# Performance work log

Measured on AMD Instinct MI355X. Metric: run time of the kernel, lower is better.

Reference implementation:

```python
import jax, jax.numpy as jnp
import numpy as np

SLOT_DIM = 256
HIDDEN = 128
NUM_REL = 8


def setup_inputs() -> dict:
    key = jax.random.key(0)
    ks = jax.random.split(key, 5)
    B, N, D = 8, 256, SLOT_DIM
    slots = jax.random.normal(ks[0], (B, N, D), dtype=jnp.float32)
    # Linear(2D -> H): store as [2D, H] (x @ W + b)
    s1 = 1.0 / np.sqrt(2 * D)
    W1 = jax.random.uniform(ks[1], (2 * D, HIDDEN), jnp.float32, -s1, s1)
    b1 = jax.random.uniform(ks[2], (HIDDEN,), jnp.float32, -s1, s1)
    s2 = 1.0 / np.sqrt(HIDDEN)
    W2 = jax.random.uniform(ks[3], (HIDDEN, NUM_REL), jnp.float32, -s2, s2)
    b2 = jax.random.uniform(ks[4], (NUM_REL,), jnp.float32, -s2, s2)
    return {"slots": slots, "W1": W1, "b1": b1, "W2": W2, "b2": b2}


def reference(slots, W1, b1, W2, b2):
    # cat([slots_i, slots_j]) @ W1 == slots_i @ W1[:D] + slots_j @ W1[D:]
    # so project each slot once, then broadcast-add over the pair grid.
    D = slots.shape[-1]
    proj_i = jnp.einsum("bnd,dh->bnh", slots, W1[:D])   # [B,N,H]
    proj_j = jnp.einsum("bnd,dh->bnh", slots, W1[D:])   # [B,N,H]
    h = proj_i[:, :, None, :] + proj_j[:, None, :, :] + b1  # [B,N,N,H]
    h = jax.nn.relu(h)
    logits = jnp.einsum("bijh,hr->bijr", h, W2) + b2     # [B,N,N,R]
    return jax.nn.sigmoid(logits)
```

## Files before the change

kernel.cpp:

```cpp
#include <hip/hip_runtime.h>
#include <hip/hip_fp16.h>
#include <math.h>

#define BATCH 8
#define NSLOT 256
#define DDIM  256
#define HID   128
#define NREL  8

typedef _Float16 half8 __attribute__((ext_vector_type(8)));
typedef float float4v __attribute__((ext_vector_type(4)));

union U8 {
  uint32_t u[4];
  _Float16 f[8];
  half8 v;
  float4 f4;
};

union H4 {
  _Float16 f[4];
  double d;
};


__global__ __launch_bounds__(256) void wt_kernel(
    const float* __restrict__ W1, _Float16* __restrict__ WT) {
  __shared__ float T[32][33];
  const int tx = threadIdx.x & 31;
  const int ty = threadIdx.x >> 5;
  const int c0 = blockIdx.x * 32, k0 = blockIdx.y * 32;
#pragma unroll
  for (int p = 0; p < 4; ++p) {
    const int k = k0 + ty + p * 8;
    const int c = c0 + tx;
    T[ty + p * 8][tx] = (c < HID) ? W1[(size_t)k * HID + c]
                                  : W1[(size_t)(DDIM + k) * HID + (c - HID)];
  }
  __syncthreads();
#pragma unroll
  for (int p = 0; p < 4; ++p) {
    const int cl = ty + p * 8;
    WT[(size_t)(c0 + cl) * 256 + k0 + tx] = (_Float16)T[tx][cl];
  }
}

__global__ __launch_bounds__(256, 4) void fused_kernel(
    const float* __restrict__ slots, const _Float16* __restrict__ WT,
    const float* __restrict__ b1, const float* __restrict__ W2,
    const float* __restrict__ b2, float* __restrict__ out) {
  __shared__ _Float16 LB[48 * 264];
  _Float16* SLI = LB;
  _Float16* SLJ = LB + 16 * 264;
  _Float16* P1L = LB;
  _Float16* P2L = LB + 16 * 136;

  const int tid  = threadIdx.x;
  const int w    = tid >> 6;
  const int lane = tid & 63;
  const int lo16 = lane & 15;
  const int kg   = lane >> 4;

  const int b  = blockIdx.z;
  const int i0 = blockIdx.y * 16;
  const int j0 = blockIdx.x * 32;
  const float* Sb = slots + (size_t)b * NSLOT * DDIM;

#pragma unroll
  for (int p = 0; p < 4; ++p) {
    const int idx = tid + p * 256;
    const int r  = idx >> 6;
    const int c4 = (idx & 63) * 4;
    const float4 f = *(const float4*)(Sb + (size_t)(i0 + r) * DDIM + c4);
    H4 h;
    h.f[0] = (_Float16)f.x; h.f[1] = (_Float16)f.y;
    h.f[2] = (_Float16)f.z; h.f[3] = (_Float16)f.w;
    *(double*)&SLI[r * 264 + c4] = h.d;
  }
#pragma unroll
  for (int p = 0; p < 8; ++p) {
    const int idx = tid + p * 256;
    const int r  = idx >> 6;
    const int c4 = (idx & 63) * 4;
    const float4 f = *(const float4*)(Sb + (size_t)(j0 + r) * DDIM + c4);
    H4 h;
    h.f[0] = (_Float16)f.x; h.f[1] = (_Float16)f.y;
    h.f[2] = (_Float16)f.z; h.f[3] = (_Float16)f.w;
    *(double*)&SLJ[r * 264 + c4] = h.d;
  }
  __syncthreads();

  float4v p1acc[2];
  float4v p2acc[2][2];
  float b1v[2];
#pragma unroll
  for (int t = 0; t < 2; ++t) {
    p1acc[t] = (float4v){0.0f, 0.0f, 0.0f, 0.0f};
    p2acc[t][0] = (float4v){0.0f, 0.0f, 0.0f, 0.0f};
    p2acc[t][1] = (float4v){0.0f, 0.0f, 0.0f, 0.0f};
  }
#pragma unroll
  for (int t = 0; t < 2; ++t) {
    const int c = (2 * w + t) * 16 + lo16;
    b1v[t] = b1[c];
    U8 bf1[8], bf2[8];
#pragma unroll
    for (int ks = 0; ks < 8; ++ks) {
      bf1[ks].f4 = *(const float4*)(WT + (size_t)c * 256 + ks * 32 + kg * 8);
      bf2[ks].f4 = *(const float4*)(WT + (size_t)(HID + c) * 256 + ks * 32 + kg * 8);
    }
#pragma unroll
    for (int ks = 0; ks < 8; ++ks) {
      U8 a;
      a.f4 = *(const float4*)&SLI[lo16 * 264 + ks * 32 + kg * 8];
      p1acc[t] = __builtin_amdgcn_mfma_f32_16x16x32_f16(a.v, bf1[ks].v, p1acc[t], 0, 0, 0);
    }
#pragma unroll
    for (int mt = 0; mt < 2; ++mt) {
#pragma unroll
      for (int ks = 0; ks < 8; ++ks) {
        U8 a;
        a.f4 = *(const float4*)&SLJ[(mt * 16 + lo16) * 264 + ks * 32 + kg * 8];
        p2acc[t][mt] =
            __builtin_amdgcn_mfma_f32_16x16x32_f16(a.v, bf2[ks].v, p2acc[t][mt], 0, 0, 0);
      }
    }
  }
  __syncthreads();

#pragma unroll
  for (int t = 0; t < 2; ++t) {
    const int col = (2 * w + t) * 16 + lo16;
#pragma unroll
    for (int reg = 0; reg < 4; ++reg) {
      P1L[(kg * 4 + reg) * 136 + col] = (_Float16)(p1acc[t][reg] + b1v[t]);
      P2L[(kg * 4 + reg) * 136 + col] = (_Float16)p2acc[t][0][reg];
      P2L[(16 + kg * 4 + reg) * 136 + col] = (_Float16)p2acc[t][1][reg];
    }
  }
  __syncthreads();

  const int n  = lo16;
  const int jw = w & 1;
  const int ih = w >> 1;

  U8 w2f[4];
#pragma unroll
  for (int kq = 0; kq < 4; ++kq) {
#pragma unroll
    for (int u = 0; u < 8; ++u) {
      const int k = kq * 32 + kg * 8 + u;
      w2f[kq].f[u] = (n < 8) ? (_Float16)W2[k * NREL + n] : (_Float16)0.0f;
    }
  }
  const float b2v = (n < 8) ? b2[n] : 0.0f;

  U8 pj[4];
#pragma unroll
  for (int kq = 0; kq < 4; ++kq) {
    pj[kq].f4 = *(const float4*)&P2L[(jw * 16 + n) * 136 + kq * 32 + kg * 8];
  }

#pragma unroll
  for (int i = 0; i < 8; ++i) {
    const int ii = ih * 8 + i;
    float4v acc = {0.0f, 0.0f, 0.0f, 0.0f};
#pragma unroll
    for (int kq = 0; kq < 4; ++kq) {
      U8 pi;
      pi.f4 = *(const float4*)&P1L[ii * 136 + kq * 32 + kg * 8];
      U8 h;
      h.v = __builtin_elementwise_max(pj[kq].v + pi.v, (half8)(_Float16)0.0f);
      acc = __builtin_amdgcn_mfma_f32_16x16x32_f16(h.v, w2f[kq].v, acc, 0, 0, 0);
    }
    if (n < 8) {
      float* obase =
          out + (((size_t)b * NSLOT + (i0 + ii)) * NSLOT + (j0 + jw * 16)) * NREL + n;
#pragma unroll
      for (int reg = 0; reg < 4; ++reg) {
        const int jrow = kg * 4 + reg;
        const float x = acc[reg] + b2v;
        obase[jrow * NREL] = __builtin_amdgcn_rcpf(1.0f + __expf(-x));
      }
    }
  }
}

extern "C" void kernel_launch(void* const* d_in, const int* in_sizes, int n_in,
                              void* d_out, int out_size, void* d_ws, size_t ws_size,
                              hipStream_t stream) {
  const float* slots = (const float*)d_in[0];
  const float* W1    = (const float*)d_in[1];
  const float* b1    = (const float*)d_in[2];
  const float* W2    = (const float*)d_in[3];
  const float* b2    = (const float*)d_in[4];
  float* out   = (float*)d_out;
  _Float16* WT = (_Float16*)d_ws;

  wt_kernel<<<dim3(8, 8), 256, 0, stream>>>(W1, WT);
  fused_kernel<<<dim3(NSLOT / 32, NSLOT / 16, BATCH), 256, 0, stream>>>(
      slots, WT, b1, W2, b2, out);
}
```

Before: 92.13 us.

## Halve j-tile to 16, double grid, and pre-transpose W2 to fp16

```diff
diff --git a/kernel.cpp b/kernel.cpp
--- a/kernel.cpp
+++ b/kernel.cpp
@@ -25,7 +25,8 @@
 
 
 __global__ __launch_bounds__(256) void wt_kernel(
-    const float* __restrict__ W1, _Float16* __restrict__ WT) {
+    const float* __restrict__ W1, const float* __restrict__ W2,
+    _Float16* __restrict__ WT, _Float16* __restrict__ W2T) {
   __shared__ float T[32][33];
   const int tx = threadIdx.x & 31;
   const int ty = threadIdx.x >> 5;
@@ -43,13 +44,21 @@
     const int cl = ty + p * 8;
     WT[(size_t)(c0 + cl) * 256 + k0 + tx] = (_Float16)T[tx][cl];
   }
+  if (blockIdx.x == 0 && blockIdx.y == 0) {
+#pragma unroll
+    for (int p = 0; p < 8; ++p) {
+      const int idx = threadIdx.x + p * 256;
+      const int n = idx >> 7, k = idx & 127;
+      W2T[n * 128 + k] = (n < 8) ? (_Float16)W2[k * NREL + n] : (_Float16)0.0f;
+    }
+  }
 }
 
 __global__ __launch_bounds__(256, 4) void fused_kernel(
     const float* __restrict__ slots, const _Float16* __restrict__ WT,
-    const float* __restrict__ b1, const float* __restrict__ W2,
+    const _Float16* __restrict__ W2T, const float* __restrict__ b1,
     const float* __restrict__ b2, float* __restrict__ out) {
-  __shared__ _Float16 LB[48 * 264];
+  __shared__ _Float16 LB[32 * 264];
   _Float16* SLI = LB;
   _Float16* SLJ = LB + 16 * 264;
   _Float16* P1L = LB;
@@ -63,41 +72,29 @@
 
   const int b  = blockIdx.z;
   const int i0 = blockIdx.y * 16;
-  const int j0 = blockIdx.x * 32;
+  const int j0 = blockIdx.x * 16;
   const float* Sb = slots + (size_t)b * NSLOT * DDIM;
 
-#pragma unroll
-  for (int p = 0; p < 4; ++p) {
-    const int idx = tid + p * 256;
-    const int r  = idx >> 6;
-    const int c4 = (idx & 63) * 4;
-    const float4 f = *(const float4*)(Sb + (size_t)(i0 + r) * DDIM + c4);
-    H4 h;
-    h.f[0] = (_Float16)f.x; h.f[1] = (_Float16)f.y;
-    h.f[2] = (_Float16)f.z; h.f[3] = (_Float16)f.w;
-    *(double*)&SLI[r * 264 + c4] = h.d;
-  }
 #pragma unroll
   for (int p = 0; p < 8; ++p) {
     const int idx = tid + p * 256;
     const int r  = idx >> 6;
     const int c4 = (idx & 63) * 4;
-    const float4 f = *(const float4*)(Sb + (size_t)(j0 + r) * DDIM + c4);
+    const int grow = (r < 16) ? (i0 + r) : (j0 + r - 16);
+    const float4 f = *(const float4*)(Sb + (size_t)grow * DDIM + c4);
     H4 h;
     h.f[0] = (_Float16)f.x; h.f[1] = (_Float16)f.y;
     h.f[2] = (_Float16)f.z; h.f[3] = (_Float16)f.w;
-    *(double*)&SLJ[r * 264 + c4] = h.d;
+    *(double*)&LB[r * 264 + c4] = h.d;
   }
   __syncthreads();
 
-  float4v p1acc[2];
-  float4v p2acc[2][2];
+  float4v p1acc[2], p2acc[2];
   float b1v[2];
 #pragma unroll
   for (int t = 0; t < 2; ++t) {
     p1acc[t] = (float4v){0.0f, 0.0f, 0.0f, 0.0f};
-    p2acc[t][0] = (float4v){0.0f, 0.0f, 0.0f, 0.0f};
-    p2acc[t][1] = (float4v){0.0f, 0.0f, 0.0f, 0.0f};
+    p2acc[t] = (float4v){0.0f, 0.0f, 0.0f, 0.0f};
   }
 #pragma unroll
   for (int t = 0; t < 2; ++t) {
@@ -116,14 +113,10 @@
       p1acc[t] = __builtin_amdgcn_mfma_f32_16x16x32_f16(a.v, bf1[ks].v, p1acc[t], 0, 0, 0);
     }
 #pragma unroll
-    for (int mt = 0; mt < 2; ++mt) {
-#pragma unroll
-      for (int ks = 0; ks < 8; ++ks) {
-        U8 a;
-        a.f4 = *(const float4*)&SLJ[(mt * 16 + lo16) * 264 + ks * 32 + kg * 8];
-        p2acc[t][mt] =
-            __builtin_amdgcn_mfma_f32_16x16x32_f16(a.v, bf2[ks].v, p2acc[t][mt], 0, 0, 0);
-      }
+    for (int ks = 0; ks < 8; ++ks) {
+      U8 a;
+      a.f4 = *(const float4*)&SLJ[lo16 * 264 + ks * 32 + kg * 8];
+      p2acc[t] = __builtin_amdgcn_mfma_f32_16x16x32_f16(a.v, bf2[ks].v, p2acc[t], 0, 0, 0);
     }
   }
   __syncthreads();
@@ -134,48 +127,37 @@
 #pragma unroll
     for (int reg = 0; reg < 4; ++reg) {
       P1L[(kg * 4 + reg) * 136 + col] = (_Float16)(p1acc[t][reg] + b1v[t]);
-      P2L[(kg * 4 + reg) * 136 + col] = (_Float16)p2acc[t][0][reg];
-      P2L[(16 + kg * 4 + reg) * 136 + col] = (_Float16)p2acc[t][1][reg];
+      P2L[(kg * 4 + reg) * 136 + col] = (_Float16)p2acc[t][reg];
     }
   }
   __syncthreads();
 
-  const int n  = lo16;
-  const int jw = w & 1;
-  const int ih = w >> 1;
-
+  const int n = lo16;
   U8 w2f[4];
 #pragma unroll
-  for (int kq = 0; kq < 4; ++kq) {
-#pragma unroll
-    for (int u = 0; u < 8; ++u) {
-      const int k = kq * 32 + kg * 8 + u;
-      w2f[kq].f[u] = (n < 8) ? (_Float16)W2[k * NREL + n] : (_Float16)0.0f;
-    }
-  }
+  for (int kq = 0; kq < 4; ++kq)
+    w2f[kq].f4 = *(const float4*)(W2T + n * 128 + kq * 32 + kg * 8);
   const float b2v = (n < 8) ? b2[n] : 0.0f;
 
   U8 pj[4];
 #pragma unroll
-  for (int kq = 0; kq < 4; ++kq) {
-    pj[kq].f4 = *(const float4*)&P2L[(jw * 16 + n) * 136 + kq * 32 + kg * 8];
-  }
+  for (int kq = 0; kq < 4; ++kq)
+    pj[kq].f4 = *(const float4*)&P2L[n * 136 + kq * 32 + kg * 8];
 
 #pragma unroll
-  for (int i = 0; i < 8; ++i) {
-    const int ii = ih * 8 + i;
+  for (int ii = 0; ii < 4; ++ii) {
+    const int i = w * 4 + ii;
     float4v acc = {0.0f, 0.0f, 0.0f, 0.0f};
 #pragma unroll
     for (int kq = 0; kq < 4; ++kq) {
       U8 pi;
-      pi.f4 = *(const float4*)&P1L[ii * 136 + kq * 32 + kg * 8];
+      pi.f4 = *(const float4*)&P1L[i * 136 + kq * 32 + kg * 8];
       U8 h;
       h.v = __builtin_elementwise_max(pj[kq].v + pi.v, (half8)(_Float16)0.0f);
       acc = __builtin_amdgcn_mfma_f32_16x16x32_f16(h.v, w2f[kq].v, acc, 0, 0, 0);
     }
     if (n < 8) {
-      float* obase =
-          out + (((size_t)b * NSLOT + (i0 + ii)) * NSLOT + (j0 + jw * 16)) * NREL + n;
+      float* obase = out + (((size_t)b * NSLOT + (i0 + i)) * NSLOT + j0) * NREL + n;
 #pragma unroll
       for (int reg = 0; reg < 4; ++reg) {
         const int jrow = kg * 4 + reg;
@@ -194,10 +176,11 @@
   const float* b1    = (const float*)d_in[2];
   const float* W2    = (const float*)d_in[3];
   const float* b2    = (const float*)d_in[4];
-  float* out   = (float*)d_out;
-  _Float16* WT = (_Float16*)d_ws;
+  float* out    = (float*)d_out;
+  _Float16* WT  = (_Float16*)d_ws;
+  _Float16* W2T = (_Float16*)((char*)d_ws + (512 << 10));
 
-  wt_kernel<<<dim3(8, 8), 256, 0, stream>>>(W1, WT);
-  fused_kernel<<<dim3(NSLOT / 32, NSLOT / 16, BATCH), 256, 0, stream>>>(
-      slots, WT, b1, W2, b2, out);
+  wt_kernel<<<dim3(8, 8), 256, 0, stream>>>(W1, W2, WT, W2T);
+  fused_kernel<<<dim3(NSLOT / 16, NSLOT / 16, BATCH), 256, 0, stream>>>(
+      slots, WT, W2T, b1, b2, out);
 }
```

After: 129.4 us. +40.5%, slower.
